# Optimization experiments

Measured on AMD Instinct MI355X. Metric: run time of the kernel, lower is better.

Reference implementation:

```python
import jax, jax.numpy as jnp
import numpy as np

TEMPERATURE = 0.1
NORM_EPS = 1e-12  # torch F.normalize clamps the norm at 1e-12


def _l2_normalize(x):
    n = jnp.sqrt(jnp.sum(x * x, axis=-1, keepdims=True))
    return x / jnp.maximum(n, NORM_EPS)


def setup_inputs() -> dict:
    key = jax.random.key(0)
    k1, k2 = jax.random.split(key)
    feat = jax.random.normal(k1, (32, 384, 28, 28), dtype=jnp.float32)
    codebook = jax.random.normal(k2, (2048, 384), dtype=jnp.float32)
    return {"feat": feat, "codebook": codebook}


def reference(feat, codebook):
    # feat: (b, c, h, w); codebook: (K, c)
    b, c, h, w = feat.shape
    K = codebook.shape[0]

    f = jnp.transpose(feat, (0, 2, 3, 1))          # (b, h, w, c), unnormalized
    flat = f.reshape(-1, c)                        # (N, c)
    flat_n = _l2_normalize(flat)                   # normalize=True
    code = _l2_normalize(codebook)                 # (K, c)

    distance = (jnp.sum(flat_n * flat_n, axis=1, keepdims=True)
                + jnp.sum(code * code, axis=1)
                - 2.0 * (flat_n @ code.T))

    # hard assignment (is_weight_sum=False): gather nearest code
    idx = jnp.argmin(distance, axis=1)             # (N,)
    q = code[idx]                                  # (N, c) == one_hot(idx) @ code
    q = q.reshape(b, h, w, c)

    # straight-through: gradient flows to f, not the quantized values
    q_feat = f + jax.lax.stop_gradient(q - f)      # (b, h, w, c)
    q_feat = jnp.transpose(q_feat, (0, 3, 1, 2))   # (b, c, h, w)

    prob = jax.nn.softmax(-distance / TEMPERATURE, axis=1)  # (N, K)
    assignment = jnp.transpose(prob.reshape(b, h, w, K), (0, 3, 1, 2))  # (b, K, h, w)

    return (f, q_feat, assignment, distance)
```

## Files before the change

kernel.cpp:

```cpp
#include <hip/hip_runtime.h>

#define B_  32
#define C_  384
#define HW_ 784
#define N_  25088
#define K_  2048

#define OFF_F    0
#define OFF_Q    9633792
#define OFF_ASG  19267584
#define OFF_DIST 70647808

#define MARGIN 6e-3f

typedef unsigned short u16;
typedef __attribute__((ext_vector_type(8))) short short8;
typedef __attribute__((ext_vector_type(4))) float floatx4;

static __device__ __forceinline__ u16 f2bf(float x) {
    unsigned u = __builtin_bit_cast(unsigned, x);
    unsigned r = (u + 0x7FFFu + ((u >> 16) & 1u)) >> 16;
    return (u16)r;
}

static __device__ __forceinline__ void gload_lds16(const void* g, void* l) {
    __builtin_amdgcn_global_load_lds(
        (const __attribute__((address_space(1))) unsigned int*)g,
        (__attribute__((address_space(3))) unsigned int*)l,
        16, 0, 0);
}

__global__ __launch_bounds__(256) void k_code(const float* __restrict__ cb,
                                              float* __restrict__ code_n,
                                              u16* __restrict__ b_hi) {
    int row  = blockIdx.x * 4 + (threadIdx.x >> 6);
    int lane = threadIdx.x & 63;
    const float* src = cb + (size_t)row * C_;
    float v[6];
    float ss = 0.f;
#pragma unroll
    for (int i = 0; i < 6; ++i) { v[i] = src[lane + 64 * i]; ss += v[i] * v[i]; }
#pragma unroll
    for (int off = 32; off; off >>= 1) ss += __shfl_xor(ss, off, 64);
    float inv = 1.f / fmaxf(sqrtf(ss), 1e-12f);
#pragma unroll
    for (int i = 0; i < 6; ++i) {
        float vn = v[i] * inv;
        code_n[(size_t)row * C_ + lane + 64 * i] = vn;
        b_hi  [(size_t)row * C_ + lane + 64 * i] = f2bf(vn);
    }
}

__global__ __launch_bounds__(256) void k_prep(const float* __restrict__ feat,
                                              float* __restrict__ f_out,
                                              float* flatn,
                                              u16* __restrict__ a_hi) {
    __shared__ float tile[C_][17];
    __shared__ float red[16][17];
    __shared__ float s_inv[16];
    int b   = blockIdx.y;
    int hw0 = blockIdx.x * 16;
    int tid = threadIdx.x;
    int px  = tid & 15, cq = tid >> 4;

#pragma unroll
    for (int it = 0; it < 24; ++it) {
        int c = cq + 16 * it;
        tile[c][px] = feat[((size_t)(b * C_ + c)) * HW_ + hw0 + px];
    }
    __syncthreads();
    float ss = 0.f;
#pragma unroll
    for (int q = 0; q < 24; ++q) {
        float v = tile[cq + 16 * q][px];
        ss = fmaf(v, v, ss);
    }
    red[cq][px] = ss;
    __syncthreads();
    if (tid < 16) {
        float tot = 0.f;
#pragma unroll
        for (int p = 0; p < 16; ++p) tot += red[p][tid];
        s_inv[tid] = 1.f / fmaxf(sqrtf(tot), 1e-12f);
    }
    __syncthreads();

    {
        int p2 = tid >> 4, cc = tid & 15;
        size_t nbase = ((size_t)(b * HW_ + hw0 + p2)) * C_;
#pragma unroll
        for (int it = 0; it < 24; ++it) {
            int c = cc + 16 * it;
            f_out[nbase + c] = tile[c][p2];
        }
    }
    {
        float inv = s_inv[px];
#pragma unroll
        for (int it = 0; it < 24; ++it) {
            int c = cq + 16 * it;
            flatn[((size_t)(b * C_ + c)) * HW_ + hw0 + px] = tile[c][px] * inv;
        }
    }
    {
        int p2 = tid >> 4, cc = tid & 15;
        float inv = s_inv[p2];
        size_t nbase = ((size_t)(b * HW_ + hw0 + p2)) * C_;
#pragma unroll
        for (int it = 0; it < 12; ++it) {
            int c0 = 2 * cc + 32 * it;
            u16 h0 = f2bf(tile[c0][p2] * inv);
            u16 h1 = f2bf(tile[c0 + 1][p2] * inv);
            unsigned pk = (unsigned)h0 | ((unsigned)h1 << 16);
            *(unsigned*)(a_hi + nbase + c0) = pk;
        }
    }
}

__global__ __launch_bounds__(256) void k_gemm(const u16* __restrict__ A,
                                              const u16* __restrict__ Bm,
                                              float* __restrict__ D) {
    __shared__ u16 As[2][128 * 32];
    __shared__ u16 Bs[2][128 * 32];
    int tid = threadIdx.x;
    int n0 = blockIdx.x * 128, m0 = blockIdx.y * 128;
    int w = tid >> 6, l = tid & 63;
    int wm = (w >> 1) * 64, wn = (w & 1) * 64;
    int q4 = l >> 4, r15 = l & 15;

    floatx4 acc[4][4];
#pragma unroll
    for (int i = 0; i < 4; ++i)
#pragma unroll
        for (int j = 0; j < 4; ++j) acc[i][j] = (floatx4)0.f;

    int srow = tid >> 2;
    int sp   = tid & 3;
    int kk0  = 8 * (sp ^ (srow & 3));

#define STAGE(buf, kt)                                                          \
    {                                                                           \
        _Pragma("unroll")                                                       \
        for (int q = 0; q < 2; ++q) {                                           \
            int row = q * 64 + srow;                                            \
            int off = (q * 256 + tid) * 16;                                     \
            gload_lds16(A  + (size_t)(m0 + row) * C_ + (kt) + kk0,              \
                        (char*)As[buf] + off);                                  \
            gload_lds16(Bm + (size_t)(n0 + row) * C_ + (kt) + kk0,              \
                        (char*)Bs[buf] + off);                                  \
        }                                                                       \
    }

    STAGE(0, 0);
    __syncthreads();

    int slot = (q4 ^ (r15 & 3)) << 4;
#pragma unroll 1
    for (int t = 0; t < 12; ++t) {
        int cur = t & 1;
        if (t < 11) STAGE(cur ^ 1, (t + 1) * 32);
        const char* Ab = (const char*)As[cur];
        const char* Bb = (const char*)Bs[cur];
        short8 a[4], b[4];
#pragma unroll
        for (int i = 0; i < 4; ++i) {
            a[i] = *(const short8*)(Ab + (wm + i * 16 + r15) * 64 + slot);
            b[i] = *(const short8*)(Bb + (wn + i * 16 + r15) * 64 + slot);
        }
#pragma unroll
        for (int i = 0; i < 4; ++i)
#pragma unroll
            for (int j = 0; j < 4; ++j)
                acc[i][j] = __builtin_amdgcn_mfma_f32_16x16x32_bf16(a[i], b[j], acc[i][j], 0, 0, 0);
        __syncthreads();
    }

#pragma unroll
    for (int i = 0; i < 4; ++i) {
        int gm = m0 + wm + i * 16 + q4 * 4;
#pragma unroll
        for (int j = 0; j < 4; ++j) {
            int gn = n0 + wn + j * 16 + r15;
            float* p = D + (size_t)gm * K_ + gn;
#pragma unroll
            for (int r = 0; r < 4; ++r)
                p[(size_t)r * K_] = 2.f - 2.f * acc[i][j][r];
        }
    }
#undef STAGE
}

__global__ __launch_bounds__(256) void k_post(const float* __restrict__ D,
                                              const float* __restrict__ code_n,
                                              const float* flatn,
                                              float* __restrict__ asg,
                                              float* q_out) {
    __shared__ float ebuf[16][260];
    __shared__ float s_dmin[16], s_inv[16];
    __shared__ int   s_amin[16], s_cnt[16], s_cand[16][32];
    int n0  = blockIdx.x * 16;
    int b   = n0 / HW_;
    int hw0 = n0 - b * HW_;
    int tid = threadIdx.x;
    int r = tid >> 4, j = tid & 15;
    const float* drow = D + (size_t)(n0 + r) * K_;
    if (j == 0) s_cnt[r] = 0;

    float lsum = 0.f, dmin = 3.4e38f;
    int   kmin = 0;
#pragma unroll 4
    for (int i = 0; i < 32; ++i) {
        int k = 4 * j + 64 * i;
        float4 dv = *(const float4*)(drow + k);
        float d0 = dv.x, d1 = dv.y, d2 = dv.z, d3 = dv.w;
        lsum += __expf(-10.f * d0) + __expf(-10.f * d1)
              + __expf(-10.f * d2) + __expf(-10.f * d3);
        if (d0 < dmin) { dmin = d0; kmin = k; }
        if (d1 < dmin) { dmin = d1; kmin = k + 1; }
        if (d2 < dmin) { dmin = d2; kmin = k + 2; }
        if (d3 < dmin) { dmin = d3; kmin = k + 3; }
    }
#pragma unroll
    for (int off = 8; off; off >>= 1) {
        float od = __shfl_xor(dmin, off, 16);
        int   ok = __shfl_xor(kmin, off, 16);
        lsum += __shfl_xor(lsum, off, 16);
        if (od < dmin || (od == dmin && ok < kmin)) { dmin = od; kmin = ok; }
    }
    if (j == 0) { s_dmin[r] = dmin; s_inv[r] = 1.f / lsum; s_amin[r] = kmin; }
    __syncthreads();

    float inv = s_inv[r], dmn = s_dmin[r];
    for (int ch = 0; ch < 8; ++ch) {
        int k0 = ch * 256;
        __syncthreads();
#pragma unroll
        for (int i = 0; i < 4; ++i) {
            int kk = 4 * j + 64 * i;
            float4 dv = *(const float4*)(drow + k0 + kk);
            float dd[4] = {dv.x, dv.y, dv.z, dv.w};
#pragma unroll
            for (int c4 = 0; c4 < 4; ++c4) {
                float d = dd[c4];
                ebuf[r][kk + c4] = __expf(-10.f * d) * inv;
                if (d <= dmn + MARGIN) {
                    int idx = atomicAdd(&s_cnt[r], 1);
                    if (idx < 32) s_cand[r][idx] = k0 + kk + c4;
                }
            }
        }
        __syncthreads();
        int px2 = tid & 15, kt = tid >> 4;
#pragma unroll
        for (int w2 = 0; w2 < 16; ++w2) {
            int kk = kt + 16 * w2;
            asg[((size_t)(b * K_ + k0 + kk)) * HW_ + hw0 + px2] = ebuf[px2][kk];
        }
    }
    __syncthreads();

    int w = tid >> 6, l = tid & 63;
    for (int t2 = 0; t2 < 4; ++t2) {
        int px  = w + 4 * t2;
        int cnt = s_cnt[px];
        if (cnt >= 2) {
            cnt = min(cnt, 32);
            float fv[6];
#pragma unroll
            for (int ii = 0; ii < 6; ++ii)
                fv[ii] = flatn[((size_t)(b * C_ + l + 64 * ii)) * HW_ + hw0 + px];
            float dbest = 3.4e38f;
            int   kbest = -1;
            for (int ci = 0; ci < cnt; ++ci) {
                int k = s_cand[px][ci];
                const float* cr = code_n + (size_t)k * C_;
                float dot = 0.f;
#pragma unroll
                for (int ii = 0; ii < 6; ++ii) dot = fmaf(fv[ii], cr[l + 64 * ii], dot);
#pragma unroll
                for (int off = 32; off; off >>= 1) dot += __shfl_xor(dot, off, 64);
                float dex = 2.f - 2.f * dot;
                bool better = (kbest < 0) || (dex < dbest) || (dex == dbest && k < kbest);
                if (better) { dbest = dex; kbest = k; }
            }
            if (l == 0) s_amin[px] = kbest;
        }
    }
    __syncthreads();

    int px2 = tid & 15, cs = tid >> 4;
#pragma unroll
    for (int it = 0; it < 24; ++it) {
        int c = cs + 16 * it;
        q_out[((size_t)(b * C_ + c)) * HW_ + hw0 + px2] = code_n[(size_t)s_amin[px2] * C_ + c];
    }
}

extern "C" void kernel_launch(void* const* d_in, const int* in_sizes, int n_in,
                              void* d_out, int out_size, void* d_ws, size_t ws_size,
                              hipStream_t stream) {
    const float* feat = (const float*)d_in[0];
    const float* cb   = (const float*)d_in[1];
    float* out    = (float*)d_out;
    float* f_out  = out + OFF_F;
    float* q_out  = out + OFF_Q;
    float* asg    = out + OFF_ASG;
    float* dist   = out + OFF_DIST;
    float* code_n = (float*)d_ws;
    u16*   a_hi   = (u16*)asg;
    u16*   b_hi   = a_hi + (size_t)N_ * C_;
    float* flatn  = q_out;

    k_code<<<K_ / 4, 256, 0, stream>>>(cb, code_n, b_hi);
    k_prep<<<dim3(HW_ / 16, B_), 256, 0, stream>>>(feat, f_out, flatn, a_hi);
    k_gemm<<<dim3(K_ / 128, N_ / 128), 256, 0, stream>>>(a_hi, b_hi, dist);
    k_post<<<N_ / 16, 256, 0, stream>>>(dist, code_n, flatn, asg, q_out);
}
```

Before: 303.6 us.

## Fuse GEMM with softmax/argmin epilogue into one kernel per 112-row tile

Merges the distance GEMM and the post-processing kernel into one kernel. Each block keeps 112 rows of A resident in LDS and streams the whole codebook through double-buffered tiles. Softmax sums and argmin are reduced in the GEMM epilogue, so the reduction pass over the distance matrix is removed. The bf16 A matrix moves into the distance output region with a 4096 row stride, and flatn is replaced by per-row inverse norms that are reapplied to feat when refining candidates. The assignment pass still rereads the distance matrix, and occupancy drops to one block per CU with 224 blocks on the device. The candidate margin is widened while the candidate cap is lowered from 32 to 16.

Result: slower. 491.7 us (+61.9%).

```diff
diff --git a/kernel.cpp b/kernel.cpp
--- a/kernel.cpp
+++ b/kernel.cpp
@@ -5,15 +5,17 @@
 #define HW_ 784
 #define N_  25088
 #define K_  2048
+#define MT  112
 
 #define OFF_F    0
 #define OFF_Q    9633792
 #define OFF_ASG  19267584
 #define OFF_DIST 70647808
 
-#define MARGIN 6e-3f
+#define MARGIN 0.02f
 
 typedef unsigned short u16;
+typedef unsigned long long u64;
 typedef __attribute__((ext_vector_type(8))) short short8;
 typedef __attribute__((ext_vector_type(4))) float floatx4;
 
@@ -53,8 +55,8 @@
 
 __global__ __launch_bounds__(256) void k_prep(const float* __restrict__ feat,
                                               float* __restrict__ f_out,
-                                              float* flatn,
-                                              u16* __restrict__ a_hi) {
+                                              float* __restrict__ inv_n,
+                                              u16* a_hi) {
     __shared__ float tile[C_][17];
     __shared__ float red[16][17];
     __shared__ float s_inv[16];
@@ -81,7 +83,9 @@
         float tot = 0.f;
 #pragma unroll
         for (int p = 0; p < 16; ++p) tot += red[p][tid];
-        s_inv[tid] = 1.f / fmaxf(sqrtf(tot), 1e-12f);
+        float inv = 1.f / fmaxf(sqrtf(tot), 1e-12f);
+        s_inv[tid] = inv;
+        inv_n[(size_t)b * HW_ + hw0 + tid] = inv;
     }
     __syncthreads();
 
@@ -95,204 +99,234 @@
         }
     }
     {
-        float inv = s_inv[px];
-#pragma unroll
-        for (int it = 0; it < 24; ++it) {
-            int c = cq + 16 * it;
-            flatn[((size_t)(b * C_ + c)) * HW_ + hw0 + px] = tile[c][px] * inv;
-        }
-    }
-    {
         int p2 = tid >> 4, cc = tid & 15;
         float inv = s_inv[p2];
-        size_t nbase = ((size_t)(b * HW_ + hw0 + p2)) * C_;
+        u16* aptr = a_hi + ((size_t)(b * HW_ + hw0 + p2)) * 4096;
 #pragma unroll
         for (int it = 0; it < 12; ++it) {
             int c0 = 2 * cc + 32 * it;
             u16 h0 = f2bf(tile[c0][p2] * inv);
             u16 h1 = f2bf(tile[c0 + 1][p2] * inv);
-            unsigned pk = (unsigned)h0 | ((unsigned)h1 << 16);
-            *(unsigned*)(a_hi + nbase + c0) = pk;
-        }
-    }
-}
-
-__global__ __launch_bounds__(256) void k_gemm(const u16* __restrict__ A,
-                                              const u16* __restrict__ Bm,
-                                              float* __restrict__ D) {
-    __shared__ u16 As[2][128 * 32];
-    __shared__ u16 Bs[2][128 * 32];
-    int tid = threadIdx.x;
-    int n0 = blockIdx.x * 128, m0 = blockIdx.y * 128;
-    int w = tid >> 6, l = tid & 63;
-    int wm = (w >> 1) * 64, wn = (w & 1) * 64;
-    int q4 = l >> 4, r15 = l & 15;
-
-    floatx4 acc[4][4];
-#pragma unroll
-    for (int i = 0; i < 4; ++i)
+            *(unsigned*)(aptr + c0) = (unsigned)h0 | ((unsigned)h1 << 16);
+        }
+    }
+}
+
+#define STAGE_B(p, it_, t_)                                                       \
+    {                                                                             \
+        _Pragma("unroll")                                                         \
+        for (int g = 0; g < 4; ++g) {                                             \
+            int v = g * 256 + tid;                                                \
+            int row = v >> 2, sp = v & 3;                                         \
+            int fs = (row ^ (row >> 2)) & 3;                                      \
+            gload_lds16(bHi + (size_t)((it_) * 256 + row) * C_ + (t_) * 32 + 8 * (sp ^ fs), \
+                        sB[p] + v * 16);                                          \
+        }                                                                         \
+    }
+
+__global__ __launch_bounds__(256, 1) void k_fused(
+    const u16* __restrict__ bHi, const float* __restrict__ codeN,
+    const float* __restrict__ invN, const float* __restrict__ feat,
+    float* dist, float* __restrict__ asg, float* __restrict__ qOut) {
+
+    __shared__ __align__(16) char sA[12 * MT * 64];
+    __shared__ __align__(16) char sB[2][256 * 64];
+    __shared__ float s_wsum[4][MT];
+    __shared__ u64   s_wmin[4][MT];
+    __shared__ float s_inv[MT], s_dmin[MT];
+    __shared__ int   s_amin[MT], s_cnt[MT], s_cand[MT][16];
+
+    const int tid = threadIdx.x;
+    const int n0  = blockIdx.x * MT;
+    const int b   = n0 / HW_;
+    const int hw0 = n0 - b * HW_;
+    const int w   = tid >> 6, l = tid & 63;
+    const int q4  = l >> 4, r15 = l & 15;
+    const int wn  = w * 64;
+
+    const u16* aHi = (const u16*)dist;
+
+#pragma unroll 1
+    for (int ch = 0; ch < 12; ++ch) {
+        for (int v = tid; v < MT * 4; v += 256) {
+            int row = v >> 2, sp = v & 3;
+            int fs = (row ^ (row >> 2)) & 3;
+            gload_lds16(aHi + (size_t)(n0 + row) * 4096 + ch * 32 + 8 * (sp ^ fs),
+                        sA + ch * (MT * 64) + v * 16);
+        }
+    }
+    STAGE_B(0, 0, 0);
+    if (tid < MT) {
+        s_wsum[0][tid] = s_wsum[1][tid] = s_wsum[2][tid] = s_wsum[3][tid] = 0.f;
+        s_wmin[0][tid] = s_wmin[1][tid] = s_wmin[2][tid] = s_wmin[3][tid] = ~0ull;
+        s_cnt[tid] = 0;
+    }
+    __syncthreads();
+
+    floatx4 acc[7][4];
+#pragma unroll
+    for (int i = 0; i < 7; ++i)
 #pragma unroll
         for (int j = 0; j < 4; ++j) acc[i][j] = (floatx4)0.f;
 
-    int srow = tid >> 2;
-    int sp   = tid & 3;
-    int kk0  = 8 * (sp ^ (srow & 3));
-
-#define STAGE(buf, kt)                                                          \
-    {                                                                           \
-        _Pragma("unroll")                                                       \
-        for (int q = 0; q < 2; ++q) {                                           \
-            int row = q * 64 + srow;                                            \
-            int off = (q * 256 + tid) * 16;                                     \
-            gload_lds16(A  + (size_t)(m0 + row) * C_ + (kt) + kk0,              \
-                        (char*)As[buf] + off);                                  \
-            gload_lds16(Bm + (size_t)(n0 + row) * C_ + (kt) + kk0,              \
-                        (char*)Bs[buf] + off);                                  \
-        }                                                                       \
-    }
-
-    STAGE(0, 0);
-    __syncthreads();
-
-    int slot = (q4 ^ (r15 & 3)) << 4;
-#pragma unroll 1
-    for (int t = 0; t < 12; ++t) {
-        int cur = t & 1;
-        if (t < 11) STAGE(cur ^ 1, (t + 1) * 32);
-        const char* Ab = (const char*)As[cur];
-        const char* Bb = (const char*)Bs[cur];
-        short8 a[4], b[4];
-#pragma unroll
-        for (int i = 0; i < 4; ++i) {
-            a[i] = *(const short8*)(Ab + (wm + i * 16 + r15) * 64 + slot);
-            b[i] = *(const short8*)(Bb + (wn + i * 16 + r15) * 64 + slot);
-        }
-#pragma unroll
-        for (int i = 0; i < 4; ++i)
+    const int slot = (q4 ^ ((r15 ^ (r15 >> 2)) & 3)) << 4;
+
+#pragma unroll 1
+    for (int c = 0; c < 96; ++c) {
+        int p = c & 1;
+        if (c < 95) {
+            int cn = c + 1;
+            STAGE_B(cn & 1, cn / 12, cn % 12);
+        }
+        const char* Ab = sA + (c % 12) * (MT * 64);
+        const char* Bb = sB[p];
+        short8 af[7], bf[4];
+#pragma unroll
+        for (int i = 0; i < 7; ++i)
+            af[i] = *(const short8*)(Ab + (i * 16 + r15) * 64 + slot);
+#pragma unroll
+        for (int j = 0; j < 4; ++j)
+            bf[j] = *(const short8*)(Bb + (wn + j * 16 + r15) * 64 + slot);
+#pragma unroll
+        for (int i = 0; i < 7; ++i)
 #pragma unroll
             for (int j = 0; j < 4; ++j)
-                acc[i][j] = __builtin_amdgcn_mfma_f32_16x16x32_bf16(a[i], b[j], acc[i][j], 0, 0, 0);
+                acc[i][j] = __builtin_amdgcn_mfma_f32_16x16x32_bf16(af[i], bf[j], acc[i][j], 0, 0, 0);
+
+        if ((c % 12) == 11) {
+            int iter = c / 12;
+#pragma unroll
+            for (int i = 0; i < 7; ++i) {
+#pragma unroll
+                for (int rr = 0; rr < 4; ++rr) {
+                    int row = i * 16 + q4 * 4 + rr;
+                    float esum = 0.f;
+                    u64 mk = ~0ull;
+#pragma unroll
+                    for (int j = 0; j < 4; ++j) {
+                        float d = 2.f - 2.f * acc[i][j][rr];
+                        int col = iter * 256 + wn + j * 16 + r15;
+                        dist[(size_t)(n0 + row) * K_ + col] = d;
+                        esum += __expf(-10.f * d);
+                        unsigned bits = __builtin_bit_cast(unsigned, d);
+                        unsigned key = bits ^ (unsigned)(((int)bits >> 31) | (int)0x80000000);
+                        u64 pk = ((u64)key << 32) | (unsigned)col;
+                        mk = pk < mk ? pk : mk;
+                    }
+#pragma unroll
+                    for (int off = 1; off < 16; off <<= 1) {
+                        esum += __shfl_xor(esum, off, 64);
+                        u64 om = __shfl_xor(mk, off, 64);
+                        mk = om < mk ? om : mk;
+                    }
+                    if (r15 == 0) {
+                        s_wsum[w][row] += esum;
+                        u64 cur = s_wmin[w][row];
+                        s_wmin[w][row] = mk < cur ? mk : cur;
+                    }
+                }
+#pragma unroll
+                for (int j = 0; j < 4; ++j) acc[i][j] = (floatx4)0.f;
+            }
+        }
         __syncthreads();
     }
 
-#pragma unroll
-    for (int i = 0; i < 4; ++i) {
-        int gm = m0 + wm + i * 16 + q4 * 4;
-#pragma unroll
-        for (int j = 0; j < 4; ++j) {
-            int gn = n0 + wn + j * 16 + r15;
-            float* p = D + (size_t)gm * K_ + gn;
-#pragma unroll
-            for (int r = 0; r < 4; ++r)
-                p[(size_t)r * K_] = 2.f - 2.f * acc[i][j][r];
-        }
-    }
-#undef STAGE
-}
-
-__global__ __launch_bounds__(256) void k_post(const float* __restrict__ D,
-                                              const float* __restrict__ code_n,
-                                              const float* flatn,
-                                              float* __restrict__ asg,
-                                              float* q_out) {
-    __shared__ float ebuf[16][260];
-    __shared__ float s_dmin[16], s_inv[16];
-    __shared__ int   s_amin[16], s_cnt[16], s_cand[16][32];
-    int n0  = blockIdx.x * 16;
-    int b   = n0 / HW_;
-    int hw0 = n0 - b * HW_;
-    int tid = threadIdx.x;
-    int r = tid >> 4, j = tid & 15;
-    const float* drow = D + (size_t)(n0 + r) * K_;
-    if (j == 0) s_cnt[r] = 0;
-
-    float lsum = 0.f, dmin = 3.4e38f;
-    int   kmin = 0;
-#pragma unroll 4
-    for (int i = 0; i < 32; ++i) {
-        int k = 4 * j + 64 * i;
-        float4 dv = *(const float4*)(drow + k);
-        float d0 = dv.x, d1 = dv.y, d2 = dv.z, d3 = dv.w;
-        lsum += __expf(-10.f * d0) + __expf(-10.f * d1)
-              + __expf(-10.f * d2) + __expf(-10.f * d3);
-        if (d0 < dmin) { dmin = d0; kmin = k; }
-        if (d1 < dmin) { dmin = d1; kmin = k + 1; }
-        if (d2 < dmin) { dmin = d2; kmin = k + 2; }
-        if (d3 < dmin) { dmin = d3; kmin = k + 3; }
-    }
-#pragma unroll
-    for (int off = 8; off; off >>= 1) {
-        float od = __shfl_xor(dmin, off, 16);
-        int   ok = __shfl_xor(kmin, off, 16);
-        lsum += __shfl_xor(lsum, off, 16);
-        if (od < dmin || (od == dmin && ok < kmin)) { dmin = od; kmin = ok; }
-    }
-    if (j == 0) { s_dmin[r] = dmin; s_inv[r] = 1.f / lsum; s_amin[r] = kmin; }
-    __syncthreads();
-
-    float inv = s_inv[r], dmn = s_dmin[r];
-    for (int ch = 0; ch < 8; ++ch) {
-        int k0 = ch * 256;
-        __syncthreads();
-#pragma unroll
-        for (int i = 0; i < 4; ++i) {
-            int kk = 4 * j + 64 * i;
-            float4 dv = *(const float4*)(drow + k0 + kk);
+    if (tid < MT) {
+        float s = s_wsum[0][tid] + s_wsum[1][tid] + s_wsum[2][tid] + s_wsum[3][tid];
+        u64 m = s_wmin[0][tid];
+        if (s_wmin[1][tid] < m) m = s_wmin[1][tid];
+        if (s_wmin[2][tid] < m) m = s_wmin[2][tid];
+        if (s_wmin[3][tid] < m) m = s_wmin[3][tid];
+        s_inv[tid]  = 1.f / s;
+        unsigned key = (unsigned)(m >> 32);
+        unsigned bits = (key & 0x80000000u) ? (key ^ 0x80000000u) : ~key;
+        s_dmin[tid] = __builtin_bit_cast(float, bits);
+        s_amin[tid] = (int)(m & 0xffffffffu);
+    }
+    __syncthreads();
+
+    float* cbf = (float*)sA;
+    const int px = tid & 127, kg = tid >> 7;
+    const int k16 = tid & 15, rg = tid >> 4;
+#pragma unroll 1
+    for (int chk = 0; chk < 32; ++chk) {
+        int k0 = chk * 64;
+        float* cbp = cbf + (chk & 1) * (64 * 113);
+#pragma unroll
+        for (int rr = 0; rr < 7; ++rr) {
+            int r = rg + 16 * rr;
+            float4 dv = *(const float4*)(dist + (size_t)(n0 + r) * K_ + k0 + 4 * k16);
+            float inv = s_inv[r], dthr = s_dmin[r] + MARGIN;
             float dd[4] = {dv.x, dv.y, dv.z, dv.w};
 #pragma unroll
-            for (int c4 = 0; c4 < 4; ++c4) {
-                float d = dd[c4];
-                ebuf[r][kk + c4] = __expf(-10.f * d) * inv;
-                if (d <= dmn + MARGIN) {
+            for (int cc = 0; cc < 4; ++cc) {
+                cbp[(4 * k16 + cc) * 113 + r] = __expf(-10.f * dd[cc]) * inv;
+                if (dd[cc] <= dthr) {
                     int idx = atomicAdd(&s_cnt[r], 1);
-                    if (idx < 32) s_cand[r][idx] = k0 + kk + c4;
+                    if (idx < 16) s_cand[r][idx] = k0 + 4 * k16 + cc;
                 }
             }
         }
         __syncthreads();
-        int px2 = tid & 15, kt = tid >> 4;
-#pragma unroll
-        for (int w2 = 0; w2 < 16; ++w2) {
-            int kk = kt + 16 * w2;
-            asg[((size_t)(b * K_ + k0 + kk)) * HW_ + hw0 + px2] = ebuf[px2][kk];
-        }
-    }
-    __syncthreads();
-
-    int w = tid >> 6, l = tid & 63;
-    for (int t2 = 0; t2 < 4; ++t2) {
-        int px  = w + 4 * t2;
-        int cnt = s_cnt[px];
-        if (cnt >= 2) {
-            cnt = min(cnt, 32);
-            float fv[6];
-#pragma unroll
-            for (int ii = 0; ii < 6; ++ii)
-                fv[ii] = flatn[((size_t)(b * C_ + l + 64 * ii)) * HW_ + hw0 + px];
-            float dbest = 3.4e38f;
-            int   kbest = -1;
-            for (int ci = 0; ci < cnt; ++ci) {
-                int k = s_cand[px][ci];
-                const float* cr = code_n + (size_t)k * C_;
-                float dot = 0.f;
-#pragma unroll
-                for (int ii = 0; ii < 6; ++ii) dot = fmaf(fv[ii], cr[l + 64 * ii], dot);
-#pragma unroll
-                for (int off = 32; off; off >>= 1) dot += __shfl_xor(dot, off, 64);
-                float dex = 2.f - 2.f * dot;
-                bool better = (kbest < 0) || (dex < dbest) || (dex == dbest && k < kbest);
-                if (better) { dbest = dex; kbest = k; }
-            }
-            if (l == 0) s_amin[px] = kbest;
-        }
-    }
-    __syncthreads();
-
-    int px2 = tid & 15, cs = tid >> 4;
-#pragma unroll
-    for (int it = 0; it < 24; ++it) {
-        int c = cs + 16 * it;
-        q_out[((size_t)(b * C_ + c)) * HW_ + hw0 + px2] = code_n[(size_t)s_amin[px2] * C_ + c];
+        if (px < MT) {
+            size_t base = ((size_t)b * K_ + k0 + kg * 32) * HW_ + hw0 + px;
+            const float* src = cbp + (kg * 32) * 113 + px;
+#pragma unroll
+            for (int ki = 0; ki < 32; ++ki)
+                asg[base + (size_t)ki * HW_] = src[ki * 113];
+        }
+    }
+    __syncthreads();
+
+#pragma unroll 1
+    for (int r = w; r < MT; r += 4) {
+        int cnt = s_cnt[r];
+        if (cnt < 2) continue;
+        cnt = cnt > 16 ? 16 : cnt;
+        float ivn = invN[n0 + r];
+        float fv[6];
+#pragma unroll
+        for (int ii = 0; ii < 6; ++ii)
+            fv[ii] = feat[((size_t)b * C_ + l + 64 * ii) * HW_ + hw0 + r] * ivn;
+        int kbest = s_amin[r];
+        float dbest;
+        {
+            float dt = 0.f;
+            const float* cr = codeN + (size_t)kbest * C_;
+#pragma unroll
+            for (int ii = 0; ii < 6; ++ii) dt = fmaf(fv[ii], cr[l + 64 * ii], dt);
+#pragma unroll
+            for (int off = 1; off < 64; off <<= 1) dt += __shfl_xor(dt, off, 64);
+            dbest = 2.f - 2.f * dt;
+        }
+        for (int ci = 0; ci < cnt; ++ci) {
+            int k = s_cand[r][ci];
+            if (k == kbest) continue;
+            float dt = 0.f;
+            const float* cr = codeN + (size_t)k * C_;
+#pragma unroll
+            for (int ii = 0; ii < 6; ++ii) dt = fmaf(fv[ii], cr[l + 64 * ii], dt);
+#pragma unroll
+            for (int off = 1; off < 64; off <<= 1) dt += __shfl_xor(dt, off, 64);
+            float dex = 2.f - 2.f * dt;
+            if (dex < dbest || (dex == dbest && k < kbest)) { dbest = dex; kbest = k; }
+        }
+        if (l == 0) s_amin[r] = kbest;
+    }
+    __syncthreads();
+
+    if (px < MT) {
+        const float* cr = codeN + (size_t)s_amin[px] * C_ + kg * 192;
+        size_t qb = ((size_t)b * C_ + kg * 192) * HW_ + hw0 + px;
+#pragma unroll 1
+        for (int c4 = 0; c4 < 48; ++c4) {
+            float4 v = *(const float4*)(cr + 4 * c4);
+            qOut[qb + (size_t)(4 * c4 + 0) * HW_] = v.x;
+            qOut[qb + (size_t)(4 * c4 + 1) * HW_] = v.y;
+            qOut[qb + (size_t)(4 * c4 + 2) * HW_] = v.z;
+            qOut[qb + (size_t)(4 * c4 + 3) * HW_] = v.w;
+        }
     }
 }
 
@@ -306,13 +340,12 @@
     float* q_out  = out + OFF_Q;
     float* asg    = out + OFF_ASG;
     float* dist   = out + OFF_DIST;
+
     float* code_n = (float*)d_ws;
-    u16*   a_hi   = (u16*)asg;
-    u16*   b_hi   = a_hi + (size_t)N_ * C_;
-    float* flatn  = q_out;
+    u16*   b_hi   = (u16*)((char*)d_ws + 3145728);
+    float* inv_n  = (float*)((char*)d_ws + 4718592);
 
     k_code<<<K_ / 4, 256, 0, stream>>>(cb, code_n, b_hi);
-    k_prep<<<dim3(HW_ / 16, B_), 256, 0, stream>>>(feat, f_out, flatn, a_hi);
-    k_gemm<<<dim3(K_ / 128, N_ / 128), 256, 0, stream>>>(a_hi, b_hi, dist);
-    k_post<<<N_ / 16, 256, 0, stream>>>(dist, code_n, flatn, asg, q_out);
-}
+    k_prep<<<dim3(HW_ / 16, B_), 256, 0, stream>>>(feat, f_out, inv_n, (u16*)dist);
+    k_fused<<<N_ / MT, 256, 0, stream>>>(b_hi, code_n, inv_n, feat, dist, asg, q_out);
+}
```

## Fuse softmax sum and argmin into GEMM epilogue, split post into assignment and quantize kernels

Applied to the files above, without the earlier changes.

The GEMM epilogue now computes per-row partial exp sums and packed (distance, column) minima for each 128-column block. It writes them to a scratch area held in the q output buffer, so the post kernel no longer makes a separate pass over the distance matrix to get the normaliser and argmin. Assignment writes are retiled to 112 pixels and split four ways along K for more parallelism. Candidate refinement and the q gather move to a new kernel that recomputes normalized features from feat, so the flatn buffer is gone. The LDS swizzle also changes and the margin is widened. In exchange there are more global atomics and scratch traffic, plus an extra launch.

Measured after the change: 344.5 us. +13.5%, slower.

```diff
diff --git a/kernel.cpp b/kernel.cpp
--- a/kernel.cpp
+++ b/kernel.cpp
@@ -5,21 +5,24 @@
 #define HW_ 784
 #define N_  25088
 #define K_  2048
+#define PPX 112
 
 #define OFF_F    0
 #define OFF_Q    9633792
 #define OFF_ASG  19267584
 #define OFF_DIST 70647808
 
-#define MARGIN 6e-3f
+#define MARGIN 0.02f
 
 typedef unsigned short u16;
+typedef unsigned int u32;
+typedef unsigned long long u64;
 typedef __attribute__((ext_vector_type(8))) short short8;
 typedef __attribute__((ext_vector_type(4))) float floatx4;
 
 static __device__ __forceinline__ u16 f2bf(float x) {
-    unsigned u = __builtin_bit_cast(unsigned, x);
-    unsigned r = (u + 0x7FFFu + ((u >> 16) & 1u)) >> 16;
+    u32 u = __builtin_bit_cast(u32, x);
+    u32 r = (u + 0x7FFFu + ((u >> 16) & 1u)) >> 16;
     return (u16)r;
 }
 
@@ -28,6 +31,18 @@
         (const __attribute__((address_space(1))) unsigned int*)g,
         (__attribute__((address_space(3))) unsigned int*)l,
         16, 0, 0);
+}
+
+static __device__ __forceinline__ size_t qslot(int b, int s, int hw) {
+    return ((size_t)b * C_ + s) * HW_ + hw;
+}
+static __device__ __forceinline__ u32 dkey(float d) {
+    u32 bits = __builtin_bit_cast(u32, d);
+    return bits ^ (u32)(((int)bits >> 31) | (int)0x80000000);
+}
+static __device__ __forceinline__ float key2f(u32 key) {
+    u32 bits = (key & 0x80000000u) ? (key ^ 0x80000000u) : ~key;
+    return __builtin_bit_cast(float, bits);
 }
 
 __global__ __launch_bounds__(256) void k_code(const float* __restrict__ cb,
@@ -53,8 +68,9 @@
 
 __global__ __launch_bounds__(256) void k_prep(const float* __restrict__ feat,
                                               float* __restrict__ f_out,
-                                              float* flatn,
-                                              u16* __restrict__ a_hi) {
+                                              float* __restrict__ inv_n,
+                                              u16* __restrict__ a_hi,
+                                              u32* __restrict__ Qi) {
     __shared__ float tile[C_][17];
     __shared__ float red[16][17];
     __shared__ float s_inv[16];
@@ -81,7 +97,10 @@
         float tot = 0.f;
 #pragma unroll
         for (int p = 0; p < 16; ++p) tot += red[p][tid];
-        s_inv[tid] = 1.f / fmaxf(sqrtf(tot), 1e-12f);
+        float inv = 1.f / fmaxf(sqrtf(tot), 1e-12f);
+        s_inv[tid] = inv;
+        inv_n[(size_t)b * HW_ + hw0 + tid] = inv;
+        Qi[qslot(b, 48, hw0 + tid)] = 0;
     }
     __syncthreads();
 
@@ -95,35 +114,30 @@
         }
     }
     {
-        float inv = s_inv[px];
-#pragma unroll
-        for (int it = 0; it < 24; ++it) {
-            int c = cq + 16 * it;
-            flatn[((size_t)(b * C_ + c)) * HW_ + hw0 + px] = tile[c][px] * inv;
-        }
-    }
-    {
         int p2 = tid >> 4, cc = tid & 15;
         float inv = s_inv[p2];
-        size_t nbase = ((size_t)(b * HW_ + hw0 + p2)) * C_;
+        u16* aptr = a_hi + ((size_t)(b * HW_ + hw0 + p2)) * C_;
 #pragma unroll
         for (int it = 0; it < 12; ++it) {
             int c0 = 2 * cc + 32 * it;
             u16 h0 = f2bf(tile[c0][p2] * inv);
             u16 h1 = f2bf(tile[c0 + 1][p2] * inv);
-            unsigned pk = (unsigned)h0 | ((unsigned)h1 << 16);
-            *(unsigned*)(a_hi + nbase + c0) = pk;
+            *(u32*)(aptr + c0) = (u32)h0 | ((u32)h1 << 16);
         }
     }
 }
 
 __global__ __launch_bounds__(256) void k_gemm(const u16* __restrict__ A,
                                               const u16* __restrict__ Bm,
-                                              float* __restrict__ D) {
+                                              float* __restrict__ D,
+                                              u32* __restrict__ Qi) {
     __shared__ u16 As[2][128 * 32];
     __shared__ u16 Bs[2][128 * 32];
+    __shared__ float s_es[4][64];
+    __shared__ u64   s_mn[4][64];
     int tid = threadIdx.x;
-    int n0 = blockIdx.x * 128, m0 = blockIdx.y * 128;
+    int kp = blockIdx.x;
+    int n0 = kp * 128, m0 = blockIdx.y * 128;
     int w = tid >> 6, l = tid & 63;
     int wm = (w >> 1) * 64, wn = (w & 1) * 64;
     int q4 = l >> 4, r15 = l & 15;
@@ -136,7 +150,8 @@
 
     int srow = tid >> 2;
     int sp   = tid & 3;
-    int kk0  = 8 * (sp ^ (srow & 3));
+    int fs   = (srow ^ (srow >> 2)) & 3;
+    int kk0  = 8 * (sp ^ fs);
 
 #define STAGE(buf, kt)                                                          \
     {                                                                           \
@@ -154,7 +169,7 @@
     STAGE(0, 0);
     __syncthreads();
 
-    int slot = (q4 ^ (r15 & 3)) << 4;
+    const int slot = (q4 ^ ((r15 ^ (r15 >> 2)) & 3)) << 4;
 #pragma unroll 1
     for (int t = 0; t < 12; ++t) {
         int cur = t & 1;
@@ -177,122 +192,199 @@
 
 #pragma unroll
     for (int i = 0; i < 4; ++i) {
-        int gm = m0 + wm + i * 16 + q4 * 4;
-#pragma unroll
-        for (int j = 0; j < 4; ++j) {
-            int gn = n0 + wn + j * 16 + r15;
-            float* p = D + (size_t)gm * K_ + gn;
-#pragma unroll
-            for (int r = 0; r < 4; ++r)
-                p[(size_t)r * K_] = 2.f - 2.f * acc[i][j][r];
-        }
+#pragma unroll
+        for (int rr = 0; rr < 4; ++rr) {
+            int row_l = wm + i * 16 + q4 * 4 + rr;
+            int grow  = m0 + row_l;
+            float esum = 0.f;
+            u64 mk = ~0ull;
+#pragma unroll
+            for (int j = 0; j < 4; ++j) {
+                float d = 2.f - 2.f * acc[i][j][rr];
+                int col = n0 + wn + j * 16 + r15;
+                D[(size_t)grow * K_ + col] = d;
+                esum += __expf(-10.f * d);
+                u64 pk = ((u64)dkey(d) << 32) | (u32)col;
+                if (pk < mk) mk = pk;
+            }
+#pragma unroll
+            for (int off = 1; off < 16; off <<= 1) {
+                esum += __shfl_xor(esum, off, 16);
+                u64 om = __shfl_xor(mk, off, 16);
+                if (om < mk) mk = om;
+            }
+            if (r15 == 0) {
+                s_es[w][row_l & 63] = esum;
+                s_mn[w][row_l & 63] = mk;
+            }
+        }
+    }
+    __syncthreads();
+    if (tid < 128) {
+        int half = tid >> 6, idx = tid & 63;
+        float es = s_es[half * 2][idx] + s_es[half * 2 + 1][idx];
+        u64 mk = s_mn[half * 2][idx];
+        u64 m2 = s_mn[half * 2 + 1][idx];
+        if (m2 < mk) mk = m2;
+        int n = m0 + tid;
+        int b = n / HW_;
+        int hw = n - b * HW_;
+        Qi[qslot(b, kp,      hw)] = __builtin_bit_cast(u32, es);
+        Qi[qslot(b, 16 + kp, hw)] = (u32)(mk >> 32);
+        Qi[qslot(b, 32 + kp, hw)] = (u32)(mk & 0xffffffffu);
     }
 #undef STAGE
 }
 
 __global__ __launch_bounds__(256) void k_post(const float* __restrict__ D,
-                                              const float* __restrict__ code_n,
-                                              const float* flatn,
-                                              float* __restrict__ asg,
-                                              float* q_out) {
-    __shared__ float ebuf[16][260];
-    __shared__ float s_dmin[16], s_inv[16];
-    __shared__ int   s_amin[16], s_cnt[16], s_cand[16][32];
-    int n0  = blockIdx.x * 16;
-    int b   = n0 / HW_;
-    int hw0 = n0 - b * HW_;
-    int tid = threadIdx.x;
-    int r = tid >> 4, j = tid & 15;
-    const float* drow = D + (size_t)(n0 + r) * K_;
-    if (j == 0) s_cnt[r] = 0;
-
-    float lsum = 0.f, dmin = 3.4e38f;
-    int   kmin = 0;
-#pragma unroll 4
-    for (int i = 0; i < 32; ++i) {
-        int k = 4 * j + 64 * i;
-        float4 dv = *(const float4*)(drow + k);
-        float d0 = dv.x, d1 = dv.y, d2 = dv.z, d3 = dv.w;
-        lsum += __expf(-10.f * d0) + __expf(-10.f * d1)
-              + __expf(-10.f * d2) + __expf(-10.f * d3);
-        if (d0 < dmin) { dmin = d0; kmin = k; }
-        if (d1 < dmin) { dmin = d1; kmin = k + 1; }
-        if (d2 < dmin) { dmin = d2; kmin = k + 2; }
-        if (d3 < dmin) { dmin = d3; kmin = k + 3; }
-    }
-#pragma unroll
-    for (int off = 8; off; off >>= 1) {
-        float od = __shfl_xor(dmin, off, 16);
-        int   ok = __shfl_xor(kmin, off, 16);
-        lsum += __shfl_xor(lsum, off, 16);
-        if (od < dmin || (od == dmin && ok < kmin)) { dmin = od; kmin = ok; }
-    }
-    if (j == 0) { s_dmin[r] = dmin; s_inv[r] = 1.f / lsum; s_amin[r] = kmin; }
-    __syncthreads();
-
-    float inv = s_inv[r], dmn = s_dmin[r];
+                                              u32* __restrict__ Qi,
+                                              float* __restrict__ asg) {
+    __shared__ float s_part[48][PPX];
+    __shared__ float tbuf[64][113];
+    __shared__ float s_inv[PPX], s_thr[PPX];
+    int tile = blockIdx.x;
+    int kc   = blockIdx.y;
+    int b    = tile / 7;
+    int hw0  = (tile - b * 7) * PPX;
+    int n0   = b * HW_ + hw0;
+    int tid  = threadIdx.x;
+    const float* Qf = (const float*)Qi;
+
+#pragma unroll
+    for (int s0 = 0; s0 < 48; s0 += 2) {
+        int s = s0 + (tid >> 7);
+        int p = tid & 127;
+        if (p < PPX) s_part[s][p] = Qf[qslot(b, s, hw0 + p)];
+    }
+    __syncthreads();
+    if (tid < PPX) {
+        float es = 0.f;
+#pragma unroll
+        for (int kp = 0; kp < 16; ++kp) es += s_part[kp][tid];
+        u64 mk = ~0ull;
+#pragma unroll
+        for (int kp = 0; kp < 16; ++kp) {
+            u32 key = __builtin_bit_cast(u32, s_part[16 + kp][tid]);
+            u32 col = __builtin_bit_cast(u32, s_part[32 + kp][tid]);
+            u64 pk = ((u64)key << 32) | col;
+            if (pk < mk) mk = pk;
+        }
+        s_inv[tid] = 1.f / es;
+        s_thr[tid] = key2f((u32)(mk >> 32)) + MARGIN;
+    }
+    __syncthreads();
+
+    int r16 = tid >> 4, c4 = (tid & 15) * 4;
+    int px = tid & 127, kg = tid >> 7;
+#pragma unroll 1
     for (int ch = 0; ch < 8; ++ch) {
-        int k0 = ch * 256;
-        __syncthreads();
-#pragma unroll
-        for (int i = 0; i < 4; ++i) {
-            int kk = 4 * j + 64 * i;
-            float4 dv = *(const float4*)(drow + k0 + kk);
+        int k0 = kc * 512 + ch * 64;
+#pragma unroll
+        for (int rr = 0; rr < 7; ++rr) {
+            int row = r16 + 16 * rr;
+            float4 dv = *(const float4*)(D + (size_t)(n0 + row) * K_ + k0 + c4);
+            float inv = s_inv[row], thr = s_thr[row];
             float dd[4] = {dv.x, dv.y, dv.z, dv.w};
 #pragma unroll
-            for (int c4 = 0; c4 < 4; ++c4) {
-                float d = dd[c4];
-                ebuf[r][kk + c4] = __expf(-10.f * d) * inv;
-                if (d <= dmn + MARGIN) {
-                    int idx = atomicAdd(&s_cnt[r], 1);
-                    if (idx < 32) s_cand[r][idx] = k0 + kk + c4;
+            for (int cc = 0; cc < 4; ++cc) {
+                float d = dd[cc];
+                tbuf[c4 + cc][row] = __expf(-10.f * d) * inv;
+                if (d <= thr) {
+                    u32 idx = atomicAdd(&Qi[qslot(b, 48, hw0 + row)], 1u);
+                    if (idx < 16) Qi[qslot(b, 49 + idx, hw0 + row)] = (u32)(k0 + c4 + cc);
                 }
             }
         }
         __syncthreads();
-        int px2 = tid & 15, kt = tid >> 4;
-#pragma unroll
-        for (int w2 = 0; w2 < 16; ++w2) {
-            int kk = kt + 16 * w2;
-            asg[((size_t)(b * K_ + k0 + kk)) * HW_ + hw0 + px2] = ebuf[px2][kk];
-        }
+        if (px < PPX) {
+            size_t base = ((size_t)(b * K_ + k0 + kg * 32)) * HW_ + hw0 + px;
+#pragma unroll
+            for (int ki = 0; ki < 32; ++ki)
+                asg[base + (size_t)ki * HW_] = tbuf[kg * 32 + ki][px];
+        }
+        __syncthreads();
+    }
+}
+
+__global__ __launch_bounds__(256) void k_q(const u32* __restrict__ Qi,
+                                           const float* __restrict__ codeN,
+                                           const float* __restrict__ invN,
+                                           const float* __restrict__ feat,
+                                           float* __restrict__ qOut) {
+    __shared__ int s_amin[PPX], s_cnt[PPX], s_cand[PPX][16];
+    int tile = blockIdx.x;
+    int b    = tile / 7;
+    int hw0  = (tile - b * 7) * PPX;
+    int npix = b * HW_ + hw0;
+    int tid  = threadIdx.x;
+
+    if (tid < PPX) {
+        u64 mk = ~0ull;
+#pragma unroll
+        for (int kp = 0; kp < 16; ++kp) {
+            u32 key = Qi[qslot(b, 16 + kp, hw0 + tid)];
+            u32 col = Qi[qslot(b, 32 + kp, hw0 + tid)];
+            u64 pk = ((u64)key << 32) | col;
+            if (pk < mk) mk = pk;
+        }
+        s_amin[tid] = (int)(mk & 0xffffffffu);
+        int cnt = (int)Qi[qslot(b, 48, hw0 + tid)];
+        cnt = cnt > 16 ? 16 : cnt;
+        s_cnt[tid] = cnt;
+        for (int ci = 0; ci < cnt; ++ci)
+            s_cand[tid][ci] = (int)Qi[qslot(b, 49 + ci, hw0 + tid)];
     }
     __syncthreads();
 
     int w = tid >> 6, l = tid & 63;
-    for (int t2 = 0; t2 < 4; ++t2) {
-        int px  = w + 4 * t2;
-        int cnt = s_cnt[px];
-        if (cnt >= 2) {
-            cnt = min(cnt, 32);
-            float fv[6];
-#pragma unroll
-            for (int ii = 0; ii < 6; ++ii)
-                fv[ii] = flatn[((size_t)(b * C_ + l + 64 * ii)) * HW_ + hw0 + px];
-            float dbest = 3.4e38f;
-            int   kbest = -1;
-            for (int ci = 0; ci < cnt; ++ci) {
-                int k = s_cand[px][ci];
-                const float* cr = code_n + (size_t)k * C_;
-                float dot = 0.f;
-#pragma unroll
-                for (int ii = 0; ii < 6; ++ii) dot = fmaf(fv[ii], cr[l + 64 * ii], dot);
-#pragma unroll
-                for (int off = 32; off; off >>= 1) dot += __shfl_xor(dot, off, 64);
-                float dex = 2.f - 2.f * dot;
-                bool better = (kbest < 0) || (dex < dbest) || (dex == dbest && k < kbest);
-                if (better) { dbest = dex; kbest = k; }
-            }
-            if (l == 0) s_amin[px] = kbest;
-        }
-    }
-    __syncthreads();
-
-    int px2 = tid & 15, cs = tid >> 4;
-#pragma unroll
-    for (int it = 0; it < 24; ++it) {
-        int c = cs + 16 * it;
-        q_out[((size_t)(b * C_ + c)) * HW_ + hw0 + px2] = code_n[(size_t)s_amin[px2] * C_ + c];
+#pragma unroll 1
+    for (int r = w; r < PPX; r += 4) {
+        int cnt = s_cnt[r];
+        if (cnt < 2) continue;
+        float ivn = invN[npix + r];
+        float fv[6];
+#pragma unroll
+        for (int ii = 0; ii < 6; ++ii)
+            fv[ii] = feat[((size_t)b * C_ + l + 64 * ii) * HW_ + hw0 + r] * ivn;
+        int kbest = s_amin[r];
+        float dbest;
+        {
+            float dt = 0.f;
+            const float* cr = codeN + (size_t)kbest * C_;
+#pragma unroll
+            for (int ii = 0; ii < 6; ++ii) dt = fmaf(fv[ii], cr[l + 64 * ii], dt);
+#pragma unroll
+            for (int off = 1; off < 64; off <<= 1) dt += __shfl_xor(dt, off, 64);
+            dbest = 2.f - 2.f * dt;
+        }
+        for (int ci = 0; ci < cnt; ++ci) {
+            int k = s_cand[r][ci];
+            if (k == kbest) continue;
+            float dt = 0.f;
+            const float* cr = codeN + (size_t)k * C_;
+#pragma unroll
+            for (int ii = 0; ii < 6; ++ii) dt = fmaf(fv[ii], cr[l + 64 * ii], dt);
+#pragma unroll
+            for (int off = 1; off < 64; off <<= 1) dt += __shfl_xor(dt, off, 64);
+            float dex = 2.f - 2.f * dt;
+            if (dex < dbest || (dex == dbest && k < kbest)) { dbest = dex; kbest = k; }
+        }
+        if (l == 0) s_amin[r] = kbest;
+    }
+    __syncthreads();
+
+    int px = tid & 127, kg = tid >> 7;
+    if (px < PPX) {
+        const float* cr = codeN + (size_t)s_amin[px] * C_ + kg * 192;
+        size_t qb = ((size_t)b * C_ + kg * 192) * HW_ + hw0 + px;
+#pragma unroll 1
+        for (int c4 = 0; c4 < 48; ++c4) {
+            float4 v = *(const float4*)(cr + 4 * c4);
+            qOut[qb + (size_t)(4 * c4 + 0) * HW_] = v.x;
+            qOut[qb + (size_t)(4 * c4 + 1) * HW_] = v.y;
+            qOut[qb + (size_t)(4 * c4 + 2) * HW_] = v.z;
+            qOut[qb + (size_t)(4 * c4 + 3) * HW_] = v.w;
+        }
     }
 }
 
@@ -306,13 +398,17 @@
     float* q_out  = out + OFF_Q;
     float* asg    = out + OFF_ASG;
     float* dist   = out + OFF_DIST;
+
     float* code_n = (float*)d_ws;
-    u16*   a_hi   = (u16*)asg;
-    u16*   b_hi   = a_hi + (size_t)N_ * C_;
-    float* flatn  = q_out;
+    float* inv_n  = (float*)((char*)d_ws + 3145728);
+
+    u16* a_hi = (u16*)asg;
+    u16* b_hi = a_hi + (size_t)N_ * C_;
+    u32* Qi   = (u32*)q_out;
 
     k_code<<<K_ / 4, 256, 0, stream>>>(cb, code_n, b_hi);
-    k_prep<<<dim3(HW_ / 16, B_), 256, 0, stream>>>(feat, f_out, flatn, a_hi);
-    k_gemm<<<dim3(K_ / 128, N_ / 128), 256, 0, stream>>>(a_hi, b_hi, dist);
-    k_post<<<N_ / 16, 256, 0, stream>>>(dist, code_n, flatn, asg, q_out);
-}
+    k_prep<<<dim3(HW_ / 16, B_), 256, 0, stream>>>(feat, f_out, inv_n, a_hi, Qi);
+    k_gemm<<<dim3(K_ / 128, N_ / 128), 256, 0, stream>>>(a_hi, b_hi, dist, Qi);
+    k_post<<<dim3(224, 4), 256, 0, stream>>>(dist, Qi, asg);
+    k_q<<<224, 256, 0, stream>>>(Qi, code_n, inv_n, feat, q_out);
+}
```
